# Kernel optimization log

Hardware: AMD Instinct MI355X
Metric: run time of the kernel (lower is better)

Reference implementation:

```python
import jax, jax.numpy as jnp
import numpy as np

N = 30000      # num nodes
E = 960000     # num edges (avg degree 32)
IN_DIM = 2048  # raw input feature dim
N_EMBED = 64
N_HID1 = 32
N_HID2 = 16
NUM_ET = 64    # num edge types (relations)
NUM_BASE = 16  # num bases for basis decomposition


def setup_inputs() -> dict:
    key = jax.random.key(0)
    ks = jax.random.split(key, 14)
    x = jax.random.normal(ks[0], (N, IN_DIM), jnp.float32)
    edge_index = jax.random.randint(ks[1], (2, E), 0, N, dtype=jnp.int32)
    edge_type = jnp.sort(jax.random.randint(ks[2], (E,), 0, NUM_ET, dtype=jnp.int32))
    # range_list[r] = [start, end) of relation r's edges (edge_type is sorted)
    bounds = jnp.searchsorted(edge_type, jnp.arange(NUM_ET + 1, dtype=jnp.int32))
    range_list = jnp.stack([bounds[:-1], bounds[1:]], axis=1)
    x_norm = jax.random.uniform(ks[3], (N,), jnp.float32, 0.5, 1.5)
    s = 0.1  # param init scale
    embed = jax.random.normal(ks[4], (IN_DIM, N_EMBED), jnp.float32)  # .normal_() in reset
    basis1 = jax.random.normal(ks[5], (NUM_BASE, N_EMBED, N_HID1), jnp.float32) * s
    att1 = jax.random.normal(ks[6], (NUM_ET, NUM_BASE), jnp.float32) * s
    root1 = jax.random.normal(ks[7], (N_EMBED, N_HID1), jnp.float32) * s
    bias1 = jnp.zeros((N_HID1,), jnp.float32)
    basis2 = jax.random.normal(ks[8], (NUM_BASE, N_HID1, N_HID2), jnp.float32) * s
    att2 = jax.random.normal(ks[9], (NUM_ET, NUM_BASE), jnp.float32) * s
    root2 = jax.random.normal(ks[10], (N_HID1, N_HID2), jnp.float32) * s
    bias2 = jnp.zeros((N_HID2,), jnp.float32)
    return dict(x=x, edge_index=edge_index, edge_type=edge_type, range_list=range_list,
                x_norm=x_norm, embed=embed, basis1=basis1, att1=att1, root1=root1,
                bias1=bias1, basis2=basis2, att2=att2, root2=root2, bias2=bias2)


def rgcn_layer(x, edge_index, edge_type, basis, att, root, bias):
    # basis-decomposed relation weights: W[r] = sum_b att[r,b] * basis[b]
    W = jnp.einsum('rb,bio->rio', att, basis)            # [R, in, out]
    # transform all nodes under every relation (R small per-relation GEMMs fused)
    H = jnp.einsum('ni,rio->rno', x, W)                  # [R, N, out]
    src, dst = edge_index[0], edge_index[1]
    msg = H[edge_type, src]                              # [E, out] gather per-edge message
    agg = jax.ops.segment_sum(msg, dst, num_segments=x.shape[0])  # scatter-add to targets
    return agg + x @ root + bias


def reference(x, edge_index, edge_type, range_list, x_norm,
              embed, basis1, att1, root1, bias1, basis2, att2, root2, bias2):
    h = (x @ embed) / x_norm[:, None]                    # embed matmul + norm
    h = jax.nn.relu(rgcn_layer(h, edge_index, edge_type, basis1, att1, root1, bias1))
    h = jax.nn.relu(rgcn_layer(h, edge_index, edge_type, basis2, att2, root2, bias2))
    return h
```

## Files before the change

### kernel.cpp

```cpp
#include <hip/hip_runtime.h>
#include <hip/hip_bf16.h>

#define NN   30000
#define EE   960000
#define IND  2048
#define NEMB 64
#define NH1  32
#define NH2  16
#define NET  64
#define NB   16

typedef __bf16 bf8 __attribute__((ext_vector_type(8)));
typedef __bf16 bf4 __attribute__((ext_vector_type(4)));
typedef __bf16 bf2 __attribute__((ext_vector_type(2)));
typedef float  f4  __attribute__((ext_vector_type(4)));

#define AS3 __attribute__((address_space(3)))
#define AS1 __attribute__((address_space(1)))

__device__ __forceinline__ void gll16(const void* g, void* l) {
    __builtin_amdgcn_global_load_lds((const AS1 unsigned int*)g,
                                     (AS3 unsigned int*)l, 16, 0, 0);
}

__device__ __forceinline__ bf8 bf8_zero() {
    bf8 z;
#pragma unroll
    for (int i = 0; i < 8; i++) z[i] = (__bf16)0.0f;
    return z;
}

__global__ __launch_bounds__(256) void k_prep(const float* __restrict__ embed,
                                              const float* __restrict__ basis1,
                                              const float* __restrict__ att1,
                                              const float* __restrict__ basis2,
                                              const float* __restrict__ att2,
                                              __bf16* __restrict__ embT,
                                              __bf16* __restrict__ W1T,
                                              __bf16* __restrict__ W2T) {
    int b = blockIdx.x;
    if (b < 512) {
        int idx = b * 256 + threadIdx.x;
        int n = idx >> 11, k = idx & 2047;
        embT[idx] = (__bf16)embed[k * NEMB + n];
    } else if (b < 576) {
        int r = b - 512;
        __shared__ float a[NB];
        if (threadIdx.x < NB) a[threadIdx.x] = att1[r * NB + threadIdx.x];
        __syncthreads();
        for (int idx = threadIdx.x; idx < NH1 * NEMB; idx += 256) {
            int o = idx >> 6, i = idx & 63;
            float acc = 0.f;
#pragma unroll
            for (int bb = 0; bb < NB; bb++) acc += a[bb] * basis1[(bb * NEMB + i) * NH1 + o];
            W1T[r * (NH1 * NEMB) + idx] = (__bf16)acc;
        }
    } else {
        int r = b - 576;
        __shared__ float a[NB];
        if (threadIdx.x < NB) a[threadIdx.x] = att2[r * NB + threadIdx.x];
        __syncthreads();
        for (int idx = threadIdx.x; idx < NH2 * NH1; idx += 256) {
            int o = idx >> 5, i = idx & 31;
            float acc = 0.f;
#pragma unroll
            for (int bb = 0; bb < NB; bb++) acc += a[bb] * basis2[(bb * NH1 + i) * NH2 + o];
            W2T[r * (NH2 * NH1) + idx] = (__bf16)acc;
        }
    }
}

__global__ __launch_bounds__(256) void k_gemm(const float* __restrict__ x,
                                              const float* __restrict__ xnorm,
                                              const __bf16* __restrict__ embT,
                                              const float* __restrict__ root1,
                                              const float* __restrict__ bias1,
                                              __bf16* __restrict__ h0b,
                                              float* __restrict__ out1) {
    __shared__ __align__(16) float  As[2][32 * 128];
    __shared__ __align__(16) __bf16 Bs[2][64 * 128];
    int t = threadIdx.x;
    int wv = t >> 6, lane = t & 63;
    int l15 = lane & 15, kg = lane >> 4;
    int rowbase = blockIdx.x * 32;
    int half = lane >> 5;
    int bslot = lane & 31;
    int q16 = lane >> 4;
    int slot16 = lane & 15;
    int n = wv * 16 + l15;
    int nswz = (n & 7) << 4;
    int aswz = (l15 & 7) << 4;
    f4 acc0 = (f4)0.0f, acc1 = (f4)0.0f;

    auto STAGE = [&](int c, int buf) {
#pragma unroll
        for (int i = 0; i < 4; i++) {
            int rp = wv * 4 + i;
            int row = rp * 2 + half;
            int grow = rowbase + row;
            if (grow >= NN) grow = NN - 1;
            const char* g = (const char*)x + (size_t)grow * (IND * 4) + c * 512
                          + ((bslot * 16) ^ ((row & 7) << 4));
            gll16(g, (char*)&As[buf][0] + rp * 1024);
        }
#pragma unroll
        for (int i = 0; i < 4; i++) {
            int rp = wv * 4 + i;
            int row = rp * 4 + q16;
            const char* g = (const char*)embT + (size_t)row * (IND * 2) + c * 256
                          + ((slot16 * 16) ^ ((row & 7) << 4));
            gll16(g, (char*)&Bs[buf][0] + rp * 1024);
        }
    };

    STAGE(0, 0);
    for (int c = 0; c < 16; c++) {
        int buf = c & 1;
        if (c < 15) {
            STAGE(c + 1, buf ^ 1);
            asm volatile("s_waitcnt vmcnt(8)" ::: "memory");
        } else {
            asm volatile("s_waitcnt vmcnt(0)" ::: "memory");
        }
        __builtin_amdgcn_s_barrier();
        __builtin_amdgcn_sched_barrier(0);
        const char* bsrow  = (const char*)&Bs[buf][0] + n * 256;
        const char* asrow0 = (const char*)&As[buf][0] + l15 * 512;
        const char* asrow1 = (const char*)&As[buf][0] + (l15 + 16) * 512;
#pragma unroll
        for (int kk = 0; kk < 4; kk++) {
            int aoff = ((kk * 128 + kg * 32) ^ aswz);
            float4 lo0 = *(const float4*)(asrow0 + aoff);
            float4 hi0 = *(const float4*)(asrow0 + (aoff ^ 16));
            float4 lo1 = *(const float4*)(asrow1 + aoff);
            float4 hi1 = *(const float4*)(asrow1 + (aoff ^ 16));
            bf8 b = *(const bf8*)(bsrow + ((kk * 64 + kg * 16) ^ nswz));
            bf8 a0, a1;
            a0[0]=(__bf16)lo0.x; a0[1]=(__bf16)lo0.y; a0[2]=(__bf16)lo0.z; a0[3]=(__bf16)lo0.w;
            a0[4]=(__bf16)hi0.x; a0[5]=(__bf16)hi0.y; a0[6]=(__bf16)hi0.z; a0[7]=(__bf16)hi0.w;
            a1[0]=(__bf16)lo1.x; a1[1]=(__bf16)lo1.y; a1[2]=(__bf16)lo1.z; a1[3]=(__bf16)lo1.w;
            a1[4]=(__bf16)hi1.x; a1[5]=(__bf16)hi1.y; a1[6]=(__bf16)hi1.z; a1[7]=(__bf16)hi1.w;
            acc0 = __builtin_amdgcn_mfma_f32_16x16x32_bf16(a0, b, acc0, 0, 0, 0);
            acc1 = __builtin_amdgcn_mfma_f32_16x16x32_bf16(a1, b, acc1, 0, 0, 0);
        }
        __builtin_amdgcn_sched_barrier(0);
        __builtin_amdgcn_s_barrier();
    }
    __bf16* h0s = (__bf16*)&As[0][0];
#pragma unroll
    for (int j = 0; j < 4; j++) {
        int lr0 = kg * 4 + j, lr1 = lr0 + 16;
        int r0 = rowbase + lr0, r1 = rowbase + lr1;
        float v0 = 0.f, v1 = 0.f;
        if (r0 < NN) v0 = acc0[j] / xnorm[r0];
        if (r1 < NN) v1 = acc1[j] / xnorm[r1];
        __bf16 b0 = (__bf16)v0, b1 = (__bf16)v1;
        if (r0 < NN) h0b[(size_t)r0 * NEMB + n] = b0;
        if (r1 < NN) h0b[(size_t)r1 * NEMB + n] = b1;
        h0s[lr0 * NEMB + n] = b0;
        h0s[lr1 * NEMB + n] = b1;
    }
    __syncthreads();
    {
        int row = t >> 3, c0 = (t & 7) * 4;
        int grow = rowbase + row;
        if (grow < NN) {
            const __bf16* hr = h0s + row * NEMB;
            float4 acc = *(const float4*)(bias1 + c0);
#pragma unroll
            for (int k = 0; k < NEMB; k++) {
                float a = (float)hr[k];
                float4 w = *(const float4*)(root1 + k * NH1 + c0);
                acc.x += a * w.x; acc.y += a * w.y;
                acc.z += a * w.z; acc.w += a * w.w;
            }
            *(float4*)(out1 + (size_t)grow * NH1 + c0) = acc;
        }
    }
}

__global__ __launch_bounds__(256) void k_edge1(const int* __restrict__ ei,
                                               const int* __restrict__ et,
                                               const __bf16* __restrict__ h0b,
                                               const __bf16* __restrict__ W1T,
                                               float* __restrict__ out1) {
    int wave = threadIdx.x >> 6, lane = threadIdx.x & 63;
    int l15 = lane & 15, kg = lane >> 4;
    int wid = blockIdx.x * 4 + wave;
    int er0 = wid * 32 + l15, er1 = er0 + 16;
    int et0v = et[er0],  et1v = et[er1];
    int src0 = ei[er0],  src1 = ei[er1];
    int dst0 = ei[EE + er0], dst1 = ei[EE + er1];
    const __bf16* hp0 = h0b + (size_t)src0 * NEMB + kg * 8;
    const __bf16* hp1 = h0b + (size_t)src1 * NEMB + kg * 8;
    bf8 a00 = *(const bf8*)hp0;
    bf8 a01 = *(const bf8*)(hp0 + 32);
    bf8 a10 = *(const bf8*)hp1;
    bf8 a11 = *(const bf8*)(hp1 + 32);
    bf8 zero = bf8_zero();
#pragma unroll
    for (int b = 0; b < 2; b++) {
        int my_et = b ? et1v : et0v;
        int my_dst = b ? dst1 : dst0;
        bf8 a0 = b ? a10 : a00;
        bf8 a1 = b ? a11 : a01;
        f4 c0 = (f4)0.0f, c1 = (f4)0.0f;
        int pos = 0;
        while (pos < 16) {
            int r = __shfl(my_et, pos);
            unsigned long long bl = __ballot(my_et == r);
            unsigned m16 = (unsigned)(bl & 0xFFFFull);
            int run = __builtin_ctz(~(m16 >> pos));
            int end = pos + run;
            const __bf16* wb = W1T + (size_t)r * (NH1 * NEMB) + (size_t)l15 * NEMB + kg * 8;
            bf8 b00 = *(const bf8*)(wb);
            bf8 b01 = *(const bf8*)(wb + 32);
            bf8 b10 = *(const bf8*)(wb + 16 * NEMB);
            bf8 b11 = *(const bf8*)(wb + 16 * NEMB + 32);
            bool use = (l15 >= pos) && (l15 < end);
            bf8 ua0 = use ? a0 : zero;
            bf8 ua1 = use ? a1 : zero;
            c0 = __builtin_amdgcn_mfma_f32_16x16x32_bf16(ua0, b00, c0, 0, 0, 0);
            c0 = __builtin_amdgcn_mfma_f32_16x16x32_bf16(ua1, b01, c0, 0, 0, 0);
            c1 = __builtin_amdgcn_mfma_f32_16x16x32_bf16(ua0, b10, c1, 0, 0, 0);
            c1 = __builtin_amdgcn_mfma_f32_16x16x32_bf16(ua1, b11, c1, 0, 0, 0);
            pos = end;
        }
#pragma unroll
        for (int j = 0; j < 4; j++) {
            int eidx = kg * 4 + j;
            int dst = __shfl(my_dst, eidx);
            atomicAdd(out1 + (size_t)dst * NH1 + l15,      c0[j]);
            atomicAdd(out1 + (size_t)dst * NH1 + 16 + l15, c1[j]);
        }
    }
}

__global__ __launch_bounds__(256) void k_mid(const float* __restrict__ out1,
                                             const float* __restrict__ root2,
                                             const float* __restrict__ bias2,
                                             __bf16* __restrict__ h1b,
                                             float* __restrict__ out) {
    int t = threadIdx.x;
    int row = blockIdx.x * 16 + (t >> 4);
    int col = t & 15;
    const float* orow = out1 + (size_t)row * NH1;
    float h[NH1];
#pragma unroll
    for (int k = 0; k < NH1; k++) h[k] = fmaxf(orow[k], 0.f);
    bf2 hb;
    hb[0] = (__bf16)h[2 * col];
    hb[1] = (__bf16)h[2 * col + 1];
    *(bf2*)(h1b + (size_t)row * NH1 + 2 * col) = hb;
    float acc = bias2[col];
#pragma unroll
    for (int k = 0; k < NH1; k++) acc += h[k] * root2[k * NH2 + col];
    out[(size_t)row * NH2 + col] = acc;
}

__global__ __launch_bounds__(256) void k_edge2(const int* __restrict__ ei,
                                               const int* __restrict__ et,
                                               const __bf16* __restrict__ h1b,
                                               const __bf16* __restrict__ W2T,
                                               float* __restrict__ out) {
    int wave = threadIdx.x >> 6, lane = threadIdx.x & 63;
    int l15 = lane & 15, kg = lane >> 4;
    int wid = blockIdx.x * 4 + wave;
    int er0 = wid * 32 + l15, er1 = er0 + 16;
    int et0v = et[er0],  et1v = et[er1];
    int src0 = ei[er0],  src1 = ei[er1];
    int dst0 = ei[EE + er0], dst1 = ei[EE + er1];
    bf8 ab0 = *(const bf8*)(h1b + (size_t)src0 * NH1 + kg * 8);
    bf8 ab1 = *(const bf8*)(h1b + (size_t)src1 * NH1 + kg * 8);
    bf8 zero = bf8_zero();
#pragma unroll
    for (int b = 0; b < 2; b++) {
        int my_et = b ? et1v : et0v;
        int my_dst = b ? dst1 : dst0;
        bf8 a = b ? ab1 : ab0;
        f4 c = (f4)0.0f;
        int pos = 0;
        while (pos < 16) {
            int r = __shfl(my_et, pos);
            unsigned long long bl = __ballot(my_et == r);
            unsigned m16 = (unsigned)(bl & 0xFFFFull);
            int run = __builtin_ctz(~(m16 >> pos));
            int end = pos + run;
            bf8 bb = *(const bf8*)(W2T + (size_t)r * (NH2 * NH1) + (size_t)l15 * NH1 + kg * 8);
            bool use = (l15 >= pos) && (l15 < end);
            c = __builtin_amdgcn_mfma_f32_16x16x32_bf16(use ? a : zero, bb, c, 0, 0, 0);
            pos = end;
        }
#pragma unroll
        for (int j = 0; j < 4; j++) {
            int eidx = kg * 4 + j;
            int dst = __shfl(my_dst, eidx);
            atomicAdd(out + (size_t)dst * NH2 + l15, c[j]);
        }
    }
}

__global__ __launch_bounds__(256) void k_relu2(float* __restrict__ o) {
    int i = blockIdx.x * 256 + threadIdx.x;
    if (i >= NN * NH2 / 4) return;
    float4 v = ((float4*)o)[i];
    v.x = fmaxf(v.x, 0.f); v.y = fmaxf(v.y, 0.f);
    v.z = fmaxf(v.z, 0.f); v.w = fmaxf(v.w, 0.f);
    ((float4*)o)[i] = v;
}

extern "C" void kernel_launch(void* const* d_in, const int* in_sizes, int n_in,
                              void* d_out, int out_size, void* d_ws, size_t ws_size,
                              hipStream_t stream) {
    const float* x      = (const float*)d_in[0];
    const int*   ei     = (const int*)d_in[1];
    const int*   et     = (const int*)d_in[2];
    const float* xnorm  = (const float*)d_in[4];
    const float* embed  = (const float*)d_in[5];
    const float* basis1 = (const float*)d_in[6];
    const float* att1   = (const float*)d_in[7];
    const float* root1  = (const float*)d_in[8];
    const float* bias1  = (const float*)d_in[9];
    const float* basis2 = (const float*)d_in[10];
    const float* att2   = (const float*)d_in[11];
    const float* root2  = (const float*)d_in[12];
    const float* bias2  = (const float*)d_in[13];
    float* out = (float*)d_out;

    char* ws = (char*)d_ws;
    __bf16* embT = (__bf16*)(ws + 0);
    __bf16* W1T  = (__bf16*)(ws + 262144);
    __bf16* W2T  = (__bf16*)(ws + 524288);
    __bf16* h0b  = (__bf16*)(ws + 589824);
    float*  out1 = (float*) (ws + 4429824);
    __bf16* h1b  = (__bf16*)(ws + 8269824);

    k_prep <<<640,  256, 0, stream>>>(embed, basis1, att1, basis2, att2, embT, W1T, W2T);
    k_gemm <<<938,  256, 0, stream>>>(x, xnorm, embT, root1, bias1, h0b, out1);
    k_edge1<<<7500, 256, 0, stream>>>(ei, et, h0b, W1T, out1);
    k_mid  <<<1875, 256, 0, stream>>>(out1, root2, bias2, h1b, out);
    k_edge2<<<7500, 256, 0, stream>>>(ei, et, h1b, W2T, out);
    k_relu2<<<469,  256, 0, stream>>>(out);
}
```

Before: 255.1 us.

## Restructure embed GEMM to stream x from registers with LDS-resident B half

The embed GEMM now tiles 128 rows by 32 columns per 512-thread block. It stages half of the transposed embedding matrix into swizzled LDS per phase and streams x straight from global memory into registers, replacing the double-buffered async global-to-LDS pipeline. The root1 projection and bias are split out into a separate k_init1 kernel that reads h0b back. This trims LDS traffic for A and synchronisation, but x is now read twice (once per column-half block), and it adds an extra kernel launch and an h0b round-trip.

```diff
diff --git a/kernel.cpp b/kernel.cpp
--- a/kernel.cpp
+++ b/kernel.cpp
@@ -14,14 +14,6 @@
 typedef __bf16 bf4 __attribute__((ext_vector_type(4)));
 typedef __bf16 bf2 __attribute__((ext_vector_type(2)));
 typedef float  f4  __attribute__((ext_vector_type(4)));
-
-#define AS3 __attribute__((address_space(3)))
-#define AS1 __attribute__((address_space(1)))
-
-__device__ __forceinline__ void gll16(const void* g, void* l) {
-    __builtin_amdgcn_global_load_lds((const AS1 unsigned int*)g,
-                                     (AS3 unsigned int*)l, 16, 0, 0);
-}
 
 __device__ __forceinline__ bf8 bf8_zero() {
     bf8 z;
@@ -70,113 +62,81 @@
     }
 }
 
-__global__ __launch_bounds__(256) void k_gemm(const float* __restrict__ x,
+__global__ __launch_bounds__(512) void k_gemm(const float* __restrict__ x,
                                               const float* __restrict__ xnorm,
                                               const __bf16* __restrict__ embT,
-                                              const float* __restrict__ root1,
-                                              const float* __restrict__ bias1,
-                                              __bf16* __restrict__ h0b,
-                                              float* __restrict__ out1) {
-    __shared__ __align__(16) float  As[2][32 * 128];
-    __shared__ __align__(16) __bf16 Bs[2][64 * 128];
+                                              __bf16* __restrict__ h0b) {
+    __shared__ __align__(16) __bf16 Bs[1024 * 32];
     int t = threadIdx.x;
     int wv = t >> 6, lane = t & 63;
     int l15 = lane & 15, kg = lane >> 4;
-    int rowbase = blockIdx.x * 32;
-    int half = lane >> 5;
-    int bslot = lane & 31;
-    int q16 = lane >> 4;
-    int slot16 = lane & 15;
-    int n = wv * 16 + l15;
-    int nswz = (n & 7) << 4;
-    int aswz = (l15 & 7) << 4;
+    int colbase = (blockIdx.x & 1) * 32;
+    int rowbase = (blockIdx.x >> 1) * 128 + wv * 16;
+    int arow = rowbase + l15;
+    const float* xrow = x + (size_t)(arow < NN ? arow : NN - 1) * IND + kg * 8;
     f4 acc0 = (f4)0.0f, acc1 = (f4)0.0f;
 
-    auto STAGE = [&](int c, int buf) {
-#pragma unroll
-        for (int i = 0; i < 4; i++) {
-            int rp = wv * 4 + i;
-            int row = rp * 2 + half;
-            int grow = rowbase + row;
-            if (grow >= NN) grow = NN - 1;
-            const char* g = (const char*)x + (size_t)grow * (IND * 4) + c * 512
-                          + ((bslot * 16) ^ ((row & 7) << 4));
-            gll16(g, (char*)&As[buf][0] + rp * 1024);
-        }
-#pragma unroll
-        for (int i = 0; i < 4; i++) {
-            int rp = wv * 4 + i;
-            int row = rp * 4 + q16;
-            const char* g = (const char*)embT + (size_t)row * (IND * 2) + c * 256
-                          + ((slot16 * 16) ^ ((row & 7) << 4));
-            gll16(g, (char*)&Bs[buf][0] + rp * 1024);
-        }
-    };
-
-    STAGE(0, 0);
-    for (int c = 0; c < 16; c++) {
-        int buf = c & 1;
-        if (c < 15) {
-            STAGE(c + 1, buf ^ 1);
-            asm volatile("s_waitcnt vmcnt(8)" ::: "memory");
-        } else {
-            asm volatile("s_waitcnt vmcnt(0)" ::: "memory");
-        }
-        __builtin_amdgcn_s_barrier();
-        __builtin_amdgcn_sched_barrier(0);
-        const char* bsrow  = (const char*)&Bs[buf][0] + n * 256;
-        const char* asrow0 = (const char*)&As[buf][0] + l15 * 512;
-        const char* asrow1 = (const char*)&As[buf][0] + (l15 + 16) * 512;
-#pragma unroll
-        for (int kk = 0; kk < 4; kk++) {
-            int aoff = ((kk * 128 + kg * 32) ^ aswz);
-            float4 lo0 = *(const float4*)(asrow0 + aoff);
-            float4 hi0 = *(const float4*)(asrow0 + (aoff ^ 16));
-            float4 lo1 = *(const float4*)(asrow1 + aoff);
-            float4 hi1 = *(const float4*)(asrow1 + (aoff ^ 16));
-            bf8 b = *(const bf8*)(bsrow + ((kk * 64 + kg * 16) ^ nswz));
-            bf8 a0, a1;
-            a0[0]=(__bf16)lo0.x; a0[1]=(__bf16)lo0.y; a0[2]=(__bf16)lo0.z; a0[3]=(__bf16)lo0.w;
-            a0[4]=(__bf16)hi0.x; a0[5]=(__bf16)hi0.y; a0[6]=(__bf16)hi0.z; a0[7]=(__bf16)hi0.w;
-            a1[0]=(__bf16)lo1.x; a1[1]=(__bf16)lo1.y; a1[2]=(__bf16)lo1.z; a1[3]=(__bf16)lo1.w;
-            a1[4]=(__bf16)hi1.x; a1[5]=(__bf16)hi1.y; a1[6]=(__bf16)hi1.z; a1[7]=(__bf16)hi1.w;
-            acc0 = __builtin_amdgcn_mfma_f32_16x16x32_bf16(a0, b, acc0, 0, 0, 0);
-            acc1 = __builtin_amdgcn_mfma_f32_16x16x32_bf16(a1, b, acc1, 0, 0, 0);
-        }
-        __builtin_amdgcn_sched_barrier(0);
-        __builtin_amdgcn_s_barrier();
-    }
-    __bf16* h0s = (__bf16*)&As[0][0];
+#pragma unroll
+    for (int ph = 0; ph < 2; ph++) {
+        if (ph) __builtin_amdgcn_s_barrier();
+#pragma unroll
+        for (int i = 0; i < 8; i++) {
+            int idxp = i * 512 + t;
+            int kg8p = idxp & 127;
+            int col  = idxp >> 7;
+            int dst16 = kg8p * 32 + (col ^ (kg8p & 31));
+            *(bf8*)(Bs + dst16 * 8) =
+                *(const bf8*)(embT + (size_t)(colbase + col) * IND + ph * 1024 + kg8p * 8);
+        }
+        __syncthreads();
+        const float* xp = xrow + ph * 1024;
+#pragma unroll 4
+        for (int k0 = 0; k0 < 1024; k0 += 32) {
+            float4 lo = *(const float4*)(xp + k0);
+            float4 hi = *(const float4*)(xp + k0 + 4);
+            bf8 a;
+            a[0]=(__bf16)lo.x; a[1]=(__bf16)lo.y; a[2]=(__bf16)lo.z; a[3]=(__bf16)lo.w;
+            a[4]=(__bf16)hi.x; a[5]=(__bf16)hi.y; a[6]=(__bf16)hi.z; a[7]=(__bf16)hi.w;
+            int kg8p = (k0 >> 3) + kg;
+            int xr = kg8p & 31;
+            bf8 b0 = *(const bf8*)(Bs + (kg8p * 32 + (l15 ^ xr)) * 8);
+            bf8 b1 = *(const bf8*)(Bs + (kg8p * 32 + ((16 + l15) ^ xr)) * 8);
+            acc0 = __builtin_amdgcn_mfma_f32_16x16x32_bf16(a, b0, acc0, 0, 0, 0);
+            acc1 = __builtin_amdgcn_mfma_f32_16x16x32_bf16(a, b1, acc1, 0, 0, 0);
+        }
+    }
 #pragma unroll
     for (int j = 0; j < 4; j++) {
-        int lr0 = kg * 4 + j, lr1 = lr0 + 16;
-        int r0 = rowbase + lr0, r1 = rowbase + lr1;
-        float v0 = 0.f, v1 = 0.f;
-        if (r0 < NN) v0 = acc0[j] / xnorm[r0];
-        if (r1 < NN) v1 = acc1[j] / xnorm[r1];
-        __bf16 b0 = (__bf16)v0, b1 = (__bf16)v1;
-        if (r0 < NN) h0b[(size_t)r0 * NEMB + n] = b0;
-        if (r1 < NN) h0b[(size_t)r1 * NEMB + n] = b1;
-        h0s[lr0 * NEMB + n] = b0;
-        h0s[lr1 * NEMB + n] = b1;
-    }
-    __syncthreads();
-    {
-        int row = t >> 3, c0 = (t & 7) * 4;
-        int grow = rowbase + row;
-        if (grow < NN) {
-            const __bf16* hr = h0s + row * NEMB;
-            float4 acc = *(const float4*)(bias1 + c0);
-#pragma unroll
-            for (int k = 0; k < NEMB; k++) {
-                float a = (float)hr[k];
-                float4 w = *(const float4*)(root1 + k * NH1 + c0);
-                acc.x += a * w.x; acc.y += a * w.y;
-                acc.z += a * w.z; acc.w += a * w.w;
-            }
-            *(float4*)(out1 + (size_t)grow * NH1 + c0) = acc;
-        }
-    }
+        int r = rowbase + kg * 4 + j;
+        if (r < NN) {
+            float inv = 1.0f / xnorm[r];
+            h0b[(size_t)r * NEMB + colbase + l15]      = (__bf16)(acc0[j] * inv);
+            h0b[(size_t)r * NEMB + colbase + 16 + l15] = (__bf16)(acc1[j] * inv);
+        }
+    }
+}
+
+__global__ __launch_bounds__(256) void k_init1(const __bf16* __restrict__ h0b,
+                                               const float* __restrict__ root1,
+                                               const float* __restrict__ bias1,
+                                               float* __restrict__ out1) {
+    int t = threadIdx.x;
+    int row = blockIdx.x * 16 + (t >> 4);
+    int colp = (t & 15) * 2;
+    const __bf16* hr = h0b + (size_t)row * NEMB;
+    float ax = bias1[colp], ay = bias1[colp + 1];
+#pragma unroll
+    for (int kb = 0; kb < 8; kb++) {
+        bf8 hv = *(const bf8*)(hr + kb * 8);
+#pragma unroll
+        for (int j = 0; j < 8; j++) {
+            float a = (float)hv[j];
+            const float* w = root1 + (kb * 8 + j) * NH1 + colp;
+            ax += a * w[0]; ay += a * w[1];
+        }
+    }
+    float2 o; o.x = ax; o.y = ay;
+    *(float2*)(out1 + (size_t)row * NH1 + colp) = o;
 }
 
 __global__ __launch_bounds__(256) void k_edge1(const int* __restrict__ ei,
@@ -336,7 +296,8 @@
     __bf16* h1b  = (__bf16*)(ws + 8269824);
 
     k_prep <<<640,  256, 0, stream>>>(embed, basis1, att1, basis2, att2, embT, W1T, W2T);
-    k_gemm <<<938,  256, 0, stream>>>(x, xnorm, embT, root1, bias1, h0b, out1);
+    k_gemm <<<470,  512, 0, stream>>>(x, xnorm, embT, h0b);
+    k_init1<<<1875, 256, 0, stream>>>(h0b, root1, bias1, out1);
     k_edge1<<<7500, 256, 0, stream>>>(ei, et, h0b, W1T, out1);
     k_mid  <<<1875, 256, 0, stream>>>(out1, root2, bias2, h1b, out);
     k_edge2<<<7500, 256, 0, stream>>>(ei, et, h1b, W2T, out);
```

Result: slower. 278.1 us (+9.0%).

## Split embed GEMM along K into four blocks with atomic accumulation

Applied to the files above, without the earlier changes.

The x@embed GEMM is split along K into four chunks, one per block, so the grid grows from 938 to 3752 blocks, and partial sums are combined with float atomicAdd into a zeroed fp32 buffer. The zeroing is folded into k_prep as extra blocks. The xnorm division, bf16 conversion and root1 matmul move into a new k_init1h kernel. This is meant to raise occupancy and parallelism for the memory-bound 245MB read of x, at the cost of atomic traffic, an extra launch and an extra fp32 round trip, with order-dependent float summation.

```diff
diff --git a/kernel.cpp b/kernel.cpp
--- a/kernel.cpp
+++ b/kernel.cpp
@@ -37,7 +37,8 @@
                                               const float* __restrict__ att2,
                                               __bf16* __restrict__ embT,
                                               __bf16* __restrict__ W1T,
-                                              __bf16* __restrict__ W2T) {
+                                              __bf16* __restrict__ W2T,
+                                              float* __restrict__ h0f) {
     int b = blockIdx.x;
     if (b < 512) {
         int idx = b * 256 + threadIdx.x;
@@ -55,7 +56,7 @@
             for (int bb = 0; bb < NB; bb++) acc += a[bb] * basis1[(bb * NEMB + i) * NH1 + o];
             W1T[r * (NH1 * NEMB) + idx] = (__bf16)acc;
         }
-    } else {
+    } else if (b < 640) {
         int r = b - 576;
         __shared__ float a[NB];
         if (threadIdx.x < NB) a[threadIdx.x] = att2[r * NB + threadIdx.x];
@@ -67,22 +68,24 @@
             for (int bb = 0; bb < NB; bb++) acc += a[bb] * basis2[(bb * NH1 + i) * NH2 + o];
             W2T[r * (NH2 * NH1) + idx] = (__bf16)acc;
         }
+    } else {
+        f4* p = (f4*)h0f;
+        const int total = NN * NEMB / 4;
+        for (int i = (b - 640) * 256 + threadIdx.x; i < total; i += 470 * 256)
+            p[i] = (f4)0.0f;
     }
 }
 
 __global__ __launch_bounds__(256) void k_gemm(const float* __restrict__ x,
-                                              const float* __restrict__ xnorm,
                                               const __bf16* __restrict__ embT,
-                                              const float* __restrict__ root1,
-                                              const float* __restrict__ bias1,
-                                              __bf16* __restrict__ h0b,
-                                              float* __restrict__ out1) {
+                                              float* __restrict__ h0f) {
     __shared__ __align__(16) float  As[2][32 * 128];
     __shared__ __align__(16) __bf16 Bs[2][64 * 128];
     int t = threadIdx.x;
     int wv = t >> 6, lane = t & 63;
     int l15 = lane & 15, kg = lane >> 4;
-    int rowbase = blockIdx.x * 32;
+    int rowbase = (blockIdx.x >> 2) * 32;
+    int c0 = (blockIdx.x & 3) * 4;
     int half = lane >> 5;
     int bslot = lane & 31;
     int q16 = lane >> 4;
@@ -113,11 +116,12 @@
         }
     };
 
-    STAGE(0, 0);
-    for (int c = 0; c < 16; c++) {
-        int buf = c & 1;
-        if (c < 15) {
-            STAGE(c + 1, buf ^ 1);
+    STAGE(c0, 0);
+#pragma unroll
+    for (int ci = 0; ci < 4; ci++) {
+        int buf = ci & 1;
+        if (ci < 3) {
+            STAGE(c0 + ci + 1, buf ^ 1);
             asm volatile("s_waitcnt vmcnt(8)" ::: "memory");
         } else {
             asm volatile("s_waitcnt vmcnt(0)" ::: "memory");
@@ -146,37 +150,49 @@
         __builtin_amdgcn_sched_barrier(0);
         __builtin_amdgcn_s_barrier();
     }
-    __bf16* h0s = (__bf16*)&As[0][0];
 #pragma unroll
     for (int j = 0; j < 4; j++) {
-        int lr0 = kg * 4 + j, lr1 = lr0 + 16;
-        int r0 = rowbase + lr0, r1 = rowbase + lr1;
-        float v0 = 0.f, v1 = 0.f;
-        if (r0 < NN) v0 = acc0[j] / xnorm[r0];
-        if (r1 < NN) v1 = acc1[j] / xnorm[r1];
-        __bf16 b0 = (__bf16)v0, b1 = (__bf16)v1;
-        if (r0 < NN) h0b[(size_t)r0 * NEMB + n] = b0;
-        if (r1 < NN) h0b[(size_t)r1 * NEMB + n] = b1;
-        h0s[lr0 * NEMB + n] = b0;
-        h0s[lr1 * NEMB + n] = b1;
-    }
-    __syncthreads();
-    {
-        int row = t >> 3, c0 = (t & 7) * 4;
-        int grow = rowbase + row;
-        if (grow < NN) {
-            const __bf16* hr = h0s + row * NEMB;
-            float4 acc = *(const float4*)(bias1 + c0);
-#pragma unroll
-            for (int k = 0; k < NEMB; k++) {
-                float a = (float)hr[k];
-                float4 w = *(const float4*)(root1 + k * NH1 + c0);
-                acc.x += a * w.x; acc.y += a * w.y;
-                acc.z += a * w.z; acc.w += a * w.w;
-            }
-            *(float4*)(out1 + (size_t)grow * NH1 + c0) = acc;
-        }
-    }
+        int r0 = rowbase + kg * 4 + j;
+        int r1 = r0 + 16;
+        if (r0 < NN) atomicAdd(h0f + (size_t)r0 * NEMB + n, acc0[j]);
+        if (r1 < NN) atomicAdd(h0f + (size_t)r1 * NEMB + n, acc1[j]);
+    }
+}
+
+__global__ __launch_bounds__(256) void k_init1h(const float* __restrict__ h0f,
+                                                const float* __restrict__ xnorm,
+                                                const float* __restrict__ root1,
+                                                const float* __restrict__ bias1,
+                                                __bf16* __restrict__ h0b,
+                                                float* __restrict__ out1) {
+    int t = threadIdx.x;
+    int row = blockIdx.x * 16 + (t >> 4);
+    int tc = t & 15;
+    float inv = 1.0f / xnorm[row];
+    const float* hr = h0f + (size_t)row * NEMB;
+    float h[NEMB];
+#pragma unroll
+    for (int k4 = 0; k4 < 16; k4++) {
+        float4 v = *(const float4*)(hr + k4 * 4);
+        h[k4 * 4 + 0] = v.x * inv;
+        h[k4 * 4 + 1] = v.y * inv;
+        h[k4 * 4 + 2] = v.z * inv;
+        h[k4 * 4 + 3] = v.w * inv;
+    }
+    bf4 hb;
+#pragma unroll
+    for (int j = 0; j < 4; j++) hb[j] = (__bf16)h[tc * 4 + j];
+    *(bf4*)(h0b + (size_t)row * NEMB + tc * 4) = hb;
+    int colp = tc * 2;
+    float ax = bias1[colp], ay = bias1[colp + 1];
+#pragma unroll
+    for (int k = 0; k < NEMB; k++) {
+        const float* w = root1 + k * NH1 + colp;
+        ax += h[k] * w[0];
+        ay += h[k] * w[1];
+    }
+    float2 o; o.x = ax; o.y = ay;
+    *(float2*)(out1 + (size_t)row * NH1 + colp) = o;
 }
 
 __global__ __launch_bounds__(256) void k_edge1(const int* __restrict__ ei,
@@ -334,11 +350,14 @@
     __bf16* h0b  = (__bf16*)(ws + 589824);
     float*  out1 = (float*) (ws + 4429824);
     __bf16* h1b  = (__bf16*)(ws + 8269824);
-
-    k_prep <<<640,  256, 0, stream>>>(embed, basis1, att1, basis2, att2, embT, W1T, W2T);
-    k_gemm <<<938,  256, 0, stream>>>(x, xnorm, embT, root1, bias1, h0b, out1);
-    k_edge1<<<7500, 256, 0, stream>>>(ei, et, h0b, W1T, out1);
-    k_mid  <<<1875, 256, 0, stream>>>(out1, root2, bias2, h1b, out);
-    k_edge2<<<7500, 256, 0, stream>>>(ei, et, h1b, W2T, out);
-    k_relu2<<<469,  256, 0, stream>>>(out);
-}
+    float*  h0f  = (float*) (ws + 10189824);
+
+    k_prep  <<<1110, 256, 0, stream>>>(embed, basis1, att1, basis2, att2,
+                                       embT, W1T, W2T, h0f);
+    k_gemm  <<<3752, 256, 0, stream>>>(x, embT, h0f);
+    k_init1h<<<1875, 256, 0, stream>>>(h0f, xnorm, root1, bias1, h0b, out1);
+    k_edge1 <<<7500, 256, 0, stream>>>(ei, et, h0b, W1T, out1);
+    k_mid   <<<1875, 256, 0, stream>>>(out1, root2, bias2, h1b, out);
+    k_edge2 <<<7500, 256, 0, stream>>>(ei, et, h1b, W2T, out);
+    k_relu2 <<<469,  256, 0, stream>>>(out);
+}
```

Result: slower. 296.8 us (+16.3%).

## Fuse all stages into one persistent kernel with software grid barriers

Applied to the files above, without the earlier changes.

Replaces six separate launches with one persistent kernel of 1024 blocks that runs the prep, the GEMM, edge layer 1, the mid transform, edge layer 2 and the relu in sequence, separated by atomic-counter grid barriers. The aim is to remove launch gaps and tail effects between small kernels. The GEMM K-chunk is halved (32 iterations instead of 16) to fit a 32KB shared buffer so four blocks fit per CU. It relies on all 1024 blocks being co-resident, and otherwise it deadlocks; the spin barriers and the lower per-block occupancy in the edge phases may also cost time.

```diff
diff --git a/kernel.cpp b/kernel.cpp
--- a/kernel.cpp
+++ b/kernel.cpp
@@ -9,6 +9,7 @@
 #define NH2  16
 #define NET  64
 #define NB   16
+#define NBLK 1024
 
 typedef __bf16 bf8 __attribute__((ext_vector_type(8)));
 typedef __bf16 bf4 __attribute__((ext_vector_type(4)));
@@ -30,37 +31,58 @@
     return z;
 }
 
-__global__ __launch_bounds__(256) void k_prep(const float* __restrict__ embed,
-                                              const float* __restrict__ basis1,
-                                              const float* __restrict__ att1,
-                                              const float* __restrict__ basis2,
-                                              const float* __restrict__ att2,
-                                              __bf16* __restrict__ embT,
-                                              __bf16* __restrict__ W1T,
-                                              __bf16* __restrict__ W2T) {
-    int b = blockIdx.x;
+__device__ __forceinline__ void gridbar(int* bar, int target) {
+    __syncthreads();
+    if (threadIdx.x == 0) {
+        __threadfence();
+        if (atomicAdd(&bar[0], 1) == NBLK - 1) {
+            bar[0] = 0;
+            __threadfence();
+            atomicAdd(&bar[1], 1);
+        }
+        while (atomicAdd(&bar[1], 0) < target) __builtin_amdgcn_s_sleep(8);
+        __threadfence();
+    }
+    __syncthreads();
+}
+
+__global__ __launch_bounds__(256, 4) void k_mega(
+        const float* __restrict__ x, const int* __restrict__ ei, const int* __restrict__ et,
+        const float* __restrict__ xnorm, const float* __restrict__ embed,
+        const float* __restrict__ basis1, const float* __restrict__ att1,
+        const float* __restrict__ root1, const float* __restrict__ bias1,
+        const float* __restrict__ basis2, const float* __restrict__ att2,
+        const float* __restrict__ root2, const float* __restrict__ bias2,
+        __bf16* __restrict__ embT, __bf16* __restrict__ W1T, __bf16* __restrict__ W2T,
+        __bf16* __restrict__ h0b, float* __restrict__ out1, __bf16* __restrict__ h1b,
+        float* __restrict__ out, int* __restrict__ bar) {
+    __shared__ __align__(16) char smem[32768];
+    int b = blockIdx.x, t = threadIdx.x;
+    int wv = t >> 6, lane = t & 63;
+    int l15 = lane & 15, kg = lane >> 4;
+
     if (b < 512) {
-        int idx = b * 256 + threadIdx.x;
+        int idx = b * 256 + t;
         int n = idx >> 11, k = idx & 2047;
         embT[idx] = (__bf16)embed[k * NEMB + n];
     } else if (b < 576) {
         int r = b - 512;
-        __shared__ float a[NB];
-        if (threadIdx.x < NB) a[threadIdx.x] = att1[r * NB + threadIdx.x];
+        float* a = (float*)smem;
+        if (t < NB) a[t] = att1[r * NB + t];
         __syncthreads();
-        for (int idx = threadIdx.x; idx < NH1 * NEMB; idx += 256) {
+        for (int idx = t; idx < NH1 * NEMB; idx += 256) {
             int o = idx >> 6, i = idx & 63;
             float acc = 0.f;
 #pragma unroll
             for (int bb = 0; bb < NB; bb++) acc += a[bb] * basis1[(bb * NEMB + i) * NH1 + o];
             W1T[r * (NH1 * NEMB) + idx] = (__bf16)acc;
         }
-    } else {
+    } else if (b < 640) {
         int r = b - 576;
-        __shared__ float a[NB];
-        if (threadIdx.x < NB) a[threadIdx.x] = att2[r * NB + threadIdx.x];
+        float* a = (float*)smem;
+        if (t < NB) a[t] = att2[r * NB + t];
         __syncthreads();
-        for (int idx = threadIdx.x; idx < NH2 * NH1; idx += 256) {
+        for (int idx = t; idx < NH2 * NH1; idx += 256) {
             int o = idx >> 5, i = idx & 31;
             float acc = 0.f;
 #pragma unroll
@@ -68,245 +90,222 @@
             W2T[r * (NH2 * NH1) + idx] = (__bf16)acc;
         }
     }
-}
-
-__global__ __launch_bounds__(256) void k_gemm(const float* __restrict__ x,
-                                              const float* __restrict__ xnorm,
-                                              const __bf16* __restrict__ embT,
-                                              const float* __restrict__ root1,
-                                              const float* __restrict__ bias1,
-                                              __bf16* __restrict__ h0b,
-                                              float* __restrict__ out1) {
-    __shared__ __align__(16) float  As[2][32 * 128];
-    __shared__ __align__(16) __bf16 Bs[2][64 * 128];
-    int t = threadIdx.x;
-    int wv = t >> 6, lane = t & 63;
-    int l15 = lane & 15, kg = lane >> 4;
-    int rowbase = blockIdx.x * 32;
-    int half = lane >> 5;
-    int bslot = lane & 31;
-    int q16 = lane >> 4;
-    int slot16 = lane & 15;
-    int n = wv * 16 + l15;
-    int nswz = (n & 7) << 4;
-    int aswz = (l15 & 7) << 4;
-    f4 acc0 = (f4)0.0f, acc1 = (f4)0.0f;
-
-    auto STAGE = [&](int c, int buf) {
-#pragma unroll
-        for (int i = 0; i < 4; i++) {
-            int rp = wv * 4 + i;
-            int row = rp * 2 + half;
+    gridbar(bar, 1);
+
+    if (b < 938) {
+        int rowbase = b * 32;
+        int q16 = lane >> 4, slot16 = lane & 15;
+        int r8i = lane >> 3, slot8 = lane & 7;
+        int n = wv * 16 + l15;
+        int bswz = (n & 7) << 4;
+        int aswz = (l15 & 7) << 4;
+        f4 acc0 = (f4)0.0f, acc1 = (f4)0.0f;
+
+        auto STAGE = [&](int c, int buf) {
+#pragma unroll
+            for (int i = 0; i < 2; i++) {
+                int rp = wv * 2 + i;
+                int row = rp * 4 + q16;
+                int grow = rowbase + row;
+                if (grow >= NN) grow = NN - 1;
+                const char* g = (const char*)x + (size_t)grow * (IND * 4) + c * 256
+                              + ((slot16 * 16) ^ ((row & 7) << 4));
+                gll16(g, smem + buf * 8192 + rp * 1024);
+            }
+#pragma unroll
+            for (int i = 0; i < 2; i++) {
+                int rp = wv * 2 + i;
+                int row = rp * 8 + r8i;
+                const char* g = (const char*)embT + (size_t)row * (IND * 2) + c * 128
+                              + ((slot8 * 16) ^ ((row & 7) << 4));
+                gll16(g, smem + 16384 + buf * 8192 + rp * 1024);
+            }
+        };
+
+        STAGE(0, 0);
+        for (int c = 0; c < 32; c++) {
+            int buf = c & 1;
+            if (c < 31) {
+                STAGE(c + 1, buf ^ 1);
+                asm volatile("s_waitcnt vmcnt(4)" ::: "memory");
+            } else {
+                asm volatile("s_waitcnt vmcnt(0)" ::: "memory");
+            }
+            __builtin_amdgcn_s_barrier();
+            __builtin_amdgcn_sched_barrier(0);
+            const char* bufA = smem + buf * 8192;
+            const char* bufB = smem + 16384 + buf * 8192;
+            const char* bsrow = bufB + n * 128;
+            const char* ar0 = bufA + l15 * 256;
+            const char* ar1 = bufA + (l15 + 16) * 256;
+#pragma unroll
+            for (int kk = 0; kk < 2; kk++) {
+                int aoff = (kg * 32 + kk * 128) ^ aswz;
+                float4 lo0 = *(const float4*)(ar0 + aoff);
+                float4 hi0 = *(const float4*)(ar0 + (aoff ^ 16));
+                float4 lo1 = *(const float4*)(ar1 + aoff);
+                float4 hi1 = *(const float4*)(ar1 + (aoff ^ 16));
+                bf8 bb = *(const bf8*)(bsrow + ((kg * 16 + kk * 64) ^ bswz));
+                bf8 a0, a1;
+                a0[0]=(__bf16)lo0.x; a0[1]=(__bf16)lo0.y; a0[2]=(__bf16)lo0.z; a0[3]=(__bf16)lo0.w;
+                a0[4]=(__bf16)hi0.x; a0[5]=(__bf16)hi0.y; a0[6]=(__bf16)hi0.z; a0[7]=(__bf16)hi0.w;
+                a1[0]=(__bf16)lo1.x; a1[1]=(__bf16)lo1.y; a1[2]=(__bf16)lo1.z; a1[3]=(__bf16)lo1.w;
+                a1[4]=(__bf16)hi1.x; a1[5]=(__bf16)hi1.y; a1[6]=(__bf16)hi1.z; a1[7]=(__bf16)hi1.w;
+                acc0 = __builtin_amdgcn_mfma_f32_16x16x32_bf16(a0, bb, acc0, 0, 0, 0);
+                acc1 = __builtin_amdgcn_mfma_f32_16x16x32_bf16(a1, bb, acc1, 0, 0, 0);
+            }
+            __builtin_amdgcn_sched_barrier(0);
+            __builtin_amdgcn_s_barrier();
+        }
+        __bf16* h0s = (__bf16*)smem;
+#pragma unroll
+        for (int j = 0; j < 4; j++) {
+            int lr0 = kg * 4 + j, lr1 = lr0 + 16;
+            int r0 = rowbase + lr0, r1 = rowbase + lr1;
+            float v0 = 0.f, v1 = 0.f;
+            if (r0 < NN) v0 = acc0[j] / xnorm[r0];
+            if (r1 < NN) v1 = acc1[j] / xnorm[r1];
+            __bf16 b0 = (__bf16)v0, b1 = (__bf16)v1;
+            if (r0 < NN) h0b[(size_t)r0 * NEMB + n] = b0;
+            if (r1 < NN) h0b[(size_t)r1 * NEMB + n] = b1;
+            h0s[lr0 * NEMB + n] = b0;
+            h0s[lr1 * NEMB + n] = b1;
+        }
+        __syncthreads();
+        {
+            int row = t >> 3, c0 = (t & 7) * 4;
             int grow = rowbase + row;
-            if (grow >= NN) grow = NN - 1;
-            const char* g = (const char*)x + (size_t)grow * (IND * 4) + c * 512
-                          + ((bslot * 16) ^ ((row & 7) << 4));
-            gll16(g, (char*)&As[buf][0] + rp * 1024);
-        }
-#pragma unroll
-        for (int i = 0; i < 4; i++) {
-            int rp = wv * 4 + i;
-            int row = rp * 4 + q16;
-            const char* g = (const char*)embT + (size_t)row * (IND * 2) + c * 256
-                          + ((slot16 * 16) ^ ((row & 7) << 4));
-            gll16(g, (char*)&Bs[buf][0] + rp * 1024);
-        }
-    };
-
-    STAGE(0, 0);
-    for (int c = 0; c < 16; c++) {
-        int buf = c & 1;
-        if (c < 15) {
-            STAGE(c + 1, buf ^ 1);
-            asm volatile("s_waitcnt vmcnt(8)" ::: "memory");
-        } else {
-            asm volatile("s_waitcnt vmcnt(0)" ::: "memory");
-        }
-        __builtin_amdgcn_s_barrier();
-        __builtin_amdgcn_sched_barrier(0);
-        const char* bsrow  = (const char*)&Bs[buf][0] + n * 256;
-        const char* asrow0 = (const char*)&As[buf][0] + l15 * 512;
-        const char* asrow1 = (const char*)&As[buf][0] + (l15 + 16) * 512;
-#pragma unroll
-        for (int kk = 0; kk < 4; kk++) {
-            int aoff = ((kk * 128 + kg * 32) ^ aswz);
-            float4 lo0 = *(const float4*)(asrow0 + aoff);
-            float4 hi0 = *(const float4*)(asrow0 + (aoff ^ 16));
-            float4 lo1 = *(const float4*)(asrow1 + aoff);
-            float4 hi1 = *(const float4*)(asrow1 + (aoff ^ 16));
-            bf8 b = *(const bf8*)(bsrow + ((kk * 64 + kg * 16) ^ nswz));
-            bf8 a0, a1;
-            a0[0]=(__bf16)lo0.x; a0[1]=(__bf16)lo0.y; a0[2]=(__bf16)lo0.z; a0[3]=(__bf16)lo0.w;
-            a0[4]=(__bf16)hi0.x; a0[5]=(__bf16)hi0.y; a0[6]=(__bf16)hi0.z; a0[7]=(__bf16)hi0.w;
-            a1[0]=(__bf16)lo1.x; a1[1]=(__bf16)lo1.y; a1[2]=(__bf16)lo1.z; a1[3]=(__bf16)lo1.w;
-            a1[4]=(__bf16)hi1.x; a1[5]=(__bf16)hi1.y; a1[6]=(__bf16)hi1.z; a1[7]=(__bf16)hi1.w;
-            acc0 = __builtin_amdgcn_mfma_f32_16x16x32_bf16(a0, b, acc0, 0, 0, 0);
-            acc1 = __builtin_amdgcn_mfma_f32_16x16x32_bf16(a1, b, acc1, 0, 0, 0);
-        }
-        __builtin_amdgcn_sched_barrier(0);
-        __builtin_amdgcn_s_barrier();
-    }
-    __bf16* h0s = (__bf16*)&As[0][0];
-#pragma unroll
-    for (int j = 0; j < 4; j++) {
-        int lr0 = kg * 4 + j, lr1 = lr0 + 16;
-        int r0 = rowbase + lr0, r1 = rowbase + lr1;
-        float v0 = 0.f, v1 = 0.f;
-        if (r0 < NN) v0 = acc0[j] / xnorm[r0];
-        if (r1 < NN) v1 = acc1[j] / xnorm[r1];
-        __bf16 b0 = (__bf16)v0, b1 = (__bf16)v1;
-        if (r0 < NN) h0b[(size_t)r0 * NEMB + n] = b0;
-        if (r1 < NN) h0b[(size_t)r1 * NEMB + n] = b1;
-        h0s[lr0 * NEMB + n] = b0;
-        h0s[lr1 * NEMB + n] = b1;
-    }
-    __syncthreads();
+            if (grow < NN) {
+                const __bf16* hr = h0s + row * NEMB;
+                float4 acc = *(const float4*)(bias1 + c0);
+#pragma unroll
+                for (int k = 0; k < NEMB; k++) {
+                    float a = (float)hr[k];
+                    float4 w = *(const float4*)(root1 + k * NH1 + c0);
+                    acc.x += a * w.x; acc.y += a * w.y;
+                    acc.z += a * w.z; acc.w += a * w.w;
+                }
+                *(float4*)(out1 + (size_t)grow * NH1 + c0) = acc;
+            }
+        }
+    }
+    gridbar(bar, 2);
+
     {
-        int row = t >> 3, c0 = (t & 7) * 4;
-        int grow = rowbase + row;
-        if (grow < NN) {
-            const __bf16* hr = h0s + row * NEMB;
-            float4 acc = *(const float4*)(bias1 + c0);
-#pragma unroll
-            for (int k = 0; k < NEMB; k++) {
-                float a = (float)hr[k];
-                float4 w = *(const float4*)(root1 + k * NH1 + c0);
-                acc.x += a * w.x; acc.y += a * w.y;
-                acc.z += a * w.z; acc.w += a * w.w;
-            }
-            *(float4*)(out1 + (size_t)grow * NH1 + c0) = acc;
-        }
-    }
-}
-
-__global__ __launch_bounds__(256) void k_edge1(const int* __restrict__ ei,
-                                               const int* __restrict__ et,
-                                               const __bf16* __restrict__ h0b,
-                                               const __bf16* __restrict__ W1T,
-                                               float* __restrict__ out1) {
-    int wave = threadIdx.x >> 6, lane = threadIdx.x & 63;
-    int l15 = lane & 15, kg = lane >> 4;
-    int wid = blockIdx.x * 4 + wave;
-    int er0 = wid * 32 + l15, er1 = er0 + 16;
-    int et0v = et[er0],  et1v = et[er1];
-    int src0 = ei[er0],  src1 = ei[er1];
-    int dst0 = ei[EE + er0], dst1 = ei[EE + er1];
-    const __bf16* hp0 = h0b + (size_t)src0 * NEMB + kg * 8;
-    const __bf16* hp1 = h0b + (size_t)src1 * NEMB + kg * 8;
-    bf8 a00 = *(const bf8*)hp0;
-    bf8 a01 = *(const bf8*)(hp0 + 32);
-    bf8 a10 = *(const bf8*)hp1;
-    bf8 a11 = *(const bf8*)(hp1 + 32);
-    bf8 zero = bf8_zero();
-#pragma unroll
-    for (int b = 0; b < 2; b++) {
-        int my_et = b ? et1v : et0v;
-        int my_dst = b ? dst1 : dst0;
-        bf8 a0 = b ? a10 : a00;
-        bf8 a1 = b ? a11 : a01;
-        f4 c0 = (f4)0.0f, c1 = (f4)0.0f;
-        int pos = 0;
-        while (pos < 16) {
-            int r = __shfl(my_et, pos);
-            unsigned long long bl = __ballot(my_et == r);
-            unsigned m16 = (unsigned)(bl & 0xFFFFull);
-            int run = __builtin_ctz(~(m16 >> pos));
-            int end = pos + run;
-            const __bf16* wb = W1T + (size_t)r * (NH1 * NEMB) + (size_t)l15 * NEMB + kg * 8;
-            bf8 b00 = *(const bf8*)(wb);
-            bf8 b01 = *(const bf8*)(wb + 32);
-            bf8 b10 = *(const bf8*)(wb + 16 * NEMB);
-            bf8 b11 = *(const bf8*)(wb + 16 * NEMB + 32);
-            bool use = (l15 >= pos) && (l15 < end);
-            bf8 ua0 = use ? a0 : zero;
-            bf8 ua1 = use ? a1 : zero;
-            c0 = __builtin_amdgcn_mfma_f32_16x16x32_bf16(ua0, b00, c0, 0, 0, 0);
-            c0 = __builtin_amdgcn_mfma_f32_16x16x32_bf16(ua1, b01, c0, 0, 0, 0);
-            c1 = __builtin_amdgcn_mfma_f32_16x16x32_bf16(ua0, b10, c1, 0, 0, 0);
-            c1 = __builtin_amdgcn_mfma_f32_16x16x32_bf16(ua1, b11, c1, 0, 0, 0);
-            pos = end;
-        }
-#pragma unroll
-        for (int j = 0; j < 4; j++) {
-            int eidx = kg * 4 + j;
-            int dst = __shfl(my_dst, eidx);
-            atomicAdd(out1 + (size_t)dst * NH1 + l15,      c0[j]);
-            atomicAdd(out1 + (size_t)dst * NH1 + 16 + l15, c1[j]);
-        }
-    }
-}
-
-__global__ __launch_bounds__(256) void k_mid(const float* __restrict__ out1,
-                                             const float* __restrict__ root2,
-                                             const float* __restrict__ bias2,
-                                             __bf16* __restrict__ h1b,
-                                             float* __restrict__ out) {
-    int t = threadIdx.x;
-    int row = blockIdx.x * 16 + (t >> 4);
-    int col = t & 15;
-    const float* orow = out1 + (size_t)row * NH1;
-    float h[NH1];
-#pragma unroll
-    for (int k = 0; k < NH1; k++) h[k] = fmaxf(orow[k], 0.f);
-    bf2 hb;
-    hb[0] = (__bf16)h[2 * col];
-    hb[1] = (__bf16)h[2 * col + 1];
-    *(bf2*)(h1b + (size_t)row * NH1 + 2 * col) = hb;
-    float acc = bias2[col];
-#pragma unroll
-    for (int k = 0; k < NH1; k++) acc += h[k] * root2[k * NH2 + col];
-    out[(size_t)row * NH2 + col] = acc;
-}
-
-__global__ __launch_bounds__(256) void k_edge2(const int* __restrict__ ei,
-                                               const int* __restrict__ et,
-                                               const __bf16* __restrict__ h1b,
-                                               const __bf16* __restrict__ W2T,
-                                               float* __restrict__ out) {
-    int wave = threadIdx.x >> 6, lane = threadIdx.x & 63;
-    int l15 = lane & 15, kg = lane >> 4;
-    int wid = blockIdx.x * 4 + wave;
-    int er0 = wid * 32 + l15, er1 = er0 + 16;
-    int et0v = et[er0],  et1v = et[er1];
-    int src0 = ei[er0],  src1 = ei[er1];
-    int dst0 = ei[EE + er0], dst1 = ei[EE + er1];
-    bf8 ab0 = *(const bf8*)(h1b + (size_t)src0 * NH1 + kg * 8);
-    bf8 ab1 = *(const bf8*)(h1b + (size_t)src1 * NH1 + kg * 8);
-    bf8 zero = bf8_zero();
-#pragma unroll
-    for (int b = 0; b < 2; b++) {
-        int my_et = b ? et1v : et0v;
-        int my_dst = b ? dst1 : dst0;
-        bf8 a = b ? ab1 : ab0;
-        f4 c = (f4)0.0f;
-        int pos = 0;
-        while (pos < 16) {
-            int r = __shfl(my_et, pos);
-            unsigned long long bl = __ballot(my_et == r);
-            unsigned m16 = (unsigned)(bl & 0xFFFFull);
-            int run = __builtin_ctz(~(m16 >> pos));
-            int end = pos + run;
-            bf8 bb = *(const bf8*)(W2T + (size_t)r * (NH2 * NH1) + (size_t)l15 * NH1 + kg * 8);
-            bool use = (l15 >= pos) && (l15 < end);
-            c = __builtin_amdgcn_mfma_f32_16x16x32_bf16(use ? a : zero, bb, c, 0, 0, 0);
-            pos = end;
-        }
-#pragma unroll
-        for (int j = 0; j < 4; j++) {
-            int eidx = kg * 4 + j;
-            int dst = __shfl(my_dst, eidx);
-            atomicAdd(out + (size_t)dst * NH2 + l15, c[j]);
-        }
-    }
-}
-
-__global__ __launch_bounds__(256) void k_relu2(float* __restrict__ o) {
-    int i = blockIdx.x * 256 + threadIdx.x;
-    if (i >= NN * NH2 / 4) return;
-    float4 v = ((float4*)o)[i];
-    v.x = fmaxf(v.x, 0.f); v.y = fmaxf(v.y, 0.f);
-    v.z = fmaxf(v.z, 0.f); v.w = fmaxf(v.w, 0.f);
-    ((float4*)o)[i] = v;
+        bf8 zero = bf8_zero();
+        for (int wid = b * 4 + wv; wid < NN; wid += NBLK * 4) {
+            int er0 = wid * 32 + l15, er1 = er0 + 16;
+            int et0v = et[er0],  et1v = et[er1];
+            int src0 = ei[er0],  src1 = ei[er1];
+            int dst0 = ei[EE + er0], dst1 = ei[EE + er1];
+            const __bf16* hp0 = h0b + (size_t)src0 * NEMB + kg * 8;
+            const __bf16* hp1 = h0b + (size_t)src1 * NEMB + kg * 8;
+            bf8 a00 = *(const bf8*)hp0;
+            bf8 a01 = *(const bf8*)(hp0 + 32);
+            bf8 a10 = *(const bf8*)hp1;
+            bf8 a11 = *(const bf8*)(hp1 + 32);
+#pragma unroll
+            for (int s = 0; s < 2; s++) {
+                int my_et = s ? et1v : et0v;
+                int my_dst = s ? dst1 : dst0;
+                bf8 a0 = s ? a10 : a00;
+                bf8 a1 = s ? a11 : a01;
+                f4 c0 = (f4)0.0f, c1 = (f4)0.0f;
+                int pos = 0;
+                while (pos < 16) {
+                    int r = __shfl(my_et, pos);
+                    unsigned long long bl = __ballot(my_et == r);
+                    unsigned m16 = (unsigned)(bl & 0xFFFFull);
+                    int run = __builtin_ctz(~(m16 >> pos));
+                    int end = pos + run;
+                    const __bf16* wb = W1T + (size_t)r * (NH1 * NEMB) + (size_t)l15 * NEMB + kg * 8;
+                    bf8 b00 = *(const bf8*)(wb);
+                    bf8 b01 = *(const bf8*)(wb + 32);
+                    bf8 b10 = *(const bf8*)(wb + 16 * NEMB);
+                    bf8 b11 = *(const bf8*)(wb + 16 * NEMB + 32);
+                    bool use = (l15 >= pos) && (l15 < end);
+                    bf8 ua0 = use ? a0 : zero;
+                    bf8 ua1 = use ? a1 : zero;
+                    c0 = __builtin_amdgcn_mfma_f32_16x16x32_bf16(ua0, b00, c0, 0, 0, 0);
+                    c0 = __builtin_amdgcn_mfma_f32_16x16x32_bf16(ua1, b01, c0, 0, 0, 0);
+                    c1 = __builtin_amdgcn_mfma_f32_16x16x32_bf16(ua0, b10, c1, 0, 0, 0);
+                    c1 = __builtin_amdgcn_mfma_f32_16x16x32_bf16(ua1, b11, c1, 0, 0, 0);
+                    pos = end;
+                }
+#pragma unroll
+                for (int j = 0; j < 4; j++) {
+                    int eidx = kg * 4 + j;
+                    int dst = __shfl(my_dst, eidx);
+                    atomicAdd(out1 + (size_t)dst * NH1 + l15,      c0[j]);
+                    atomicAdd(out1 + (size_t)dst * NH1 + 16 + l15, c1[j]);
+                }
+            }
+        }
+    }
+    gridbar(bar, 3);
+
+    for (int rb = b; rb < 1875; rb += NBLK) {
+        int row = rb * 16 + (t >> 4);
+        int col = t & 15;
+        const float* orow = out1 + (size_t)row * NH1;
+        float h[NH1];
+#pragma unroll
+        for (int k = 0; k < NH1; k++) h[k] = fmaxf(orow[k], 0.f);
+        bf2 hb;
+        hb[0] = (__bf16)h[2 * col];
+        hb[1] = (__bf16)h[2 * col + 1];
+        *(bf2*)(h1b + (size_t)row * NH1 + 2 * col) = hb;
+        float acc = bias2[col];
+#pragma unroll
+        for (int k = 0; k < NH1; k++) acc += h[k] * root2[k * NH2 + col];
+        out[(size_t)row * NH2 + col] = acc;
+    }
+    gridbar(bar, 4);
+
+    {
+        bf8 zero = bf8_zero();
+        for (int wid = b * 4 + wv; wid < NN; wid += NBLK * 4) {
+            int er0 = wid * 32 + l15, er1 = er0 + 16;
+            int et0v = et[er0],  et1v = et[er1];
+            int src0 = ei[er0],  src1 = ei[er1];
+            int dst0 = ei[EE + er0], dst1 = ei[EE + er1];
+            bf8 ab0 = *(const bf8*)(h1b + (size_t)src0 * NH1 + kg * 8);
+            bf8 ab1 = *(const bf8*)(h1b + (size_t)src1 * NH1 + kg * 8);
+#pragma unroll
+            for (int s = 0; s < 2; s++) {
+                int my_et = s ? et1v : et0v;
+                int my_dst = s ? dst1 : dst0;
+                bf8 a = s ? ab1 : ab0;
+                f4 c = (f4)0.0f;
+                int pos = 0;
+                while (pos < 16) {
+                    int r = __shfl(my_et, pos);
+                    unsigned long long bl = __ballot(my_et == r);
+                    unsigned m16 = (unsigned)(bl & 0xFFFFull);
+                    int run = __builtin_ctz(~(m16 >> pos));
+                    int end = pos + run;
+                    bf8 bb = *(const bf8*)(W2T + (size_t)r * (NH2 * NH1) + (size_t)l15 * NH1 + kg * 8);
+                    bool use = (l15 >= pos) && (l15 < end);
+                    c = __builtin_amdgcn_mfma_f32_16x16x32_bf16(use ? a : zero, bb, c, 0, 0, 0);
+                    pos = end;
+                }
+#pragma unroll
+                for (int j = 0; j < 4; j++) {
+                    int eidx = kg * 4 + j;
+                    int dst = __shfl(my_dst, eidx);
+                    atomicAdd(out + (size_t)dst * NH2 + l15, c[j]);
+                }
+            }
+        }
+    }
+    gridbar(bar, 5);
+
+    for (int i = b * 256 + t; i < NN * NH2 / 4; i += NBLK * 256) {
+        float4 v = ((float4*)out)[i];
+        v.x = fmaxf(v.x, 0.f); v.y = fmaxf(v.y, 0.f);
+        v.z = fmaxf(v.z, 0.f); v.w = fmaxf(v.w, 0.f);
+        ((float4*)out)[i] = v;
+    }
 }
 
 extern "C" void kernel_launch(void* const* d_in, const int* in_sizes, int n_in,
@@ -334,11 +333,10 @@
     __bf16* h0b  = (__bf16*)(ws + 589824);
     float*  out1 = (float*) (ws + 4429824);
     __bf16* h1b  = (__bf16*)(ws + 8269824);
-
-    k_prep <<<640,  256, 0, stream>>>(embed, basis1, att1, basis2, att2, embT, W1T, W2T);
-    k_gemm <<<938,  256, 0, stream>>>(x, xnorm, embT, root1, bias1, h0b, out1);
-    k_edge1<<<7500, 256, 0, stream>>>(ei, et, h0b, W1T, out1);
-    k_mid  <<<1875, 256, 0, stream>>>(out1, root2, bias2, h1b, out);
-    k_edge2<<<7500, 256, 0, stream>>>(ei, et, h1b, W2T, out);
-    k_relu2<<<469,  256, 0, stream>>>(out);
-}
+    int*    bar  = (int*)   (ws + 10189824);
+
+    hipMemsetAsync(bar, 0, 64, stream);
+    k_mega<<<NBLK, 256, 0, stream>>>(x, ei, et, xnorm, embed, basis1, att1, root1, bias1,
+                                     basis2, att2, root2, bias2,
+                                     embT, W1T, W2T, h0b, out1, h1b, out, bar);
+}
```

Result: slower. 761.6 us (+198.5%).
